# Performance work log

Measured on AMD Instinct MI355X. Metric: run time of the kernel, lower is better.

## Reference

```python
import jax, jax.numpy as jnp
import numpy as np

B, C, H, W = 8, 3840, 32, 32
C8 = C // 8


def setup_inputs() -> dict:
    key = jax.random.key(0)
    ks = jax.random.split(key, 4)
    x = jax.random.normal(ks[0], (B, C, H, W), dtype=jnp.float32)
    Wq = jax.random.normal(ks[1], (C8, C), dtype=jnp.float32) * 0.02
    Wk = jax.random.normal(ks[2], (C8, C), dtype=jnp.float32) * 0.02
    Wv = jax.random.normal(ks[3], (C, C), dtype=jnp.float32) * 0.02
    bq = jnp.zeros((C8,), jnp.float32)
    bk = jnp.zeros((C8,), jnp.float32)
    bv = jnp.zeros((C,), jnp.float32)
    gamma = jnp.zeros((1,), jnp.float32)
    return {"x": x, "Wq": Wq, "bq": bq, "Wk": Wk, "bk": bk,
            "Wv": Wv, "bv": bv, "gamma": gamma}


def reference(x, Wq, bq, Wk, bk, Wv, bv, gamma):
    b, c, h, w = x.shape
    n = h * w
    xf = x.reshape(b, c, n)  # flatten spatial: (B, C, N)
    # 1x1 convs == per-pixel channel matmuls
    q = jnp.einsum('oc,bcn->bon', Wq, xf) + bq[None, :, None]   # (B, C/8, N)
    k = jnp.einsum('oc,bcn->bon', Wk, xf) + bk[None, :, None]   # (B, C/8, N)
    v = jnp.einsum('oc,bcn->bon', Wv, xf) + bv[None, :, None]   # (B, C,  N)
    # energy[b,i,j] = q[b,:,i] . k[b,:,j]  (no scaling, as in source)
    energy = jnp.einsum('bci,bcj->bij', q, k)                    # (B, N, N)
    attn = jax.nn.softmax(energy, axis=-1)
    # out[b,c,i] = sum_j v[b,c,j] * attn[b,i,j]
    out = jnp.einsum('bcj,bij->bci', v, attn).reshape(b, c, h, w)
    return out * gamma + x
```

## Files before the change

kernel.cpp:

```cpp
#include <hip/hip_runtime.h>
#include <stdint.h>


typedef __attribute__((ext_vector_type(4))) float f32x4;
typedef __attribute__((ext_vector_type(8))) short bf16x8;
typedef __attribute__((ext_vector_type(4))) short s16x4;

namespace {
constexpr int kB = 8, kC = 3840, kC8 = 480, kN = 1024;
constexpr int kM  = 4800;
constexpr int kMp = 4864;
constexpr int kNT = kB * kN;
}

__device__ __forceinline__ short f2bf(float f) {
    union { float f; uint32_t u; } v; v.f = f;
    return (short)((v.u + 0x7FFFu + ((v.u >> 16) & 1u)) >> 16);
}

__device__ __forceinline__ void gl16(const void* g, void* l) {
    __builtin_amdgcn_global_load_lds(
        (const __attribute__((address_space(1))) void*)g,
        (__attribute__((address_space(3))) void*)(uint32_t)(uintptr_t)l,
        16, 0, 0);
}

#define DSR(d, a, o) asm volatile("ds_read_b128 %0, %1 offset:" o \
    : "=v"(d) : "v"(a) : "memory")

__global__ __launch_bounds__(256)
void convert_wc(const float* __restrict__ Wq, const float* __restrict__ Wk,
                const float* __restrict__ Wv, short* __restrict__ Wc)
{
    const size_t g  = (size_t)blockIdx.x * 256 + threadIdx.x;
    const size_t e0 = g * 8;
    const int r = (int)(e0 / kC);
    const int c = (int)(e0 % kC);
    const float* src = nullptr;
    if (r < kC8)          src = Wq + (size_t)r * kC + c;
    else if (r < 2 * kC8) src = Wk + (size_t)(r - kC8) * kC + c;
    else if (r < kM)      src = Wv + (size_t)(r - 2 * kC8) * kC + c;
    bf16x8 o;
    if (src) {
        float4 a = *(const float4*)src;
        float4 b = *(const float4*)(src + 4);
        o[0]=f2bf(a.x); o[1]=f2bf(a.y); o[2]=f2bf(a.z); o[3]=f2bf(a.w);
        o[4]=f2bf(b.x); o[5]=f2bf(b.y); o[6]=f2bf(b.z); o[7]=f2bf(b.w);
    } else {
        o = (bf16x8)0;
    }
    *(bf16x8*)(Wc + e0) = o;
}

__global__ __launch_bounds__(256)
void convert_bias(const float* __restrict__ bq, const float* __restrict__ bk,
                  const float* __restrict__ bv, float* __restrict__ biasC)
{
    const int r = blockIdx.x * 256 + threadIdx.x;
    if (r >= kMp) return;
    biasC[r] = r < kC8 ? bq[r] : r < 2*kC8 ? bk[r - kC8] : r < kM ? bv[r - 2*kC8] : 0.f;
}

__global__ __launch_bounds__(256)
void transpose_x(const float* __restrict__ x, short* __restrict__ xbT)
{
    __shared__ float t[32][33];
    const int tid = threadIdx.x;
    const int b = blockIdx.z, c0 = blockIdx.y * 32, n0 = blockIdx.x * 32;
    const int r = tid >> 3, q4 = (tid & 7) * 4;
    float4 v = *(const float4*)(x + ((size_t)b * kC + c0 + r) * kN + n0 + q4);
    t[r][q4] = v.x; t[r][q4+1] = v.y; t[r][q4+2] = v.z; t[r][q4+3] = v.w;
    __syncthreads();
    s16x4 o;
    o[0] = f2bf(t[q4+0][r]); o[1] = f2bf(t[q4+1][r]);
    o[2] = f2bf(t[q4+2][r]); o[3] = f2bf(t[q4+3][r]);
    *(s16x4*)(xbT + (size_t)(b * kN + n0 + r) * kC + c0 + q4) = o;
}

__global__ __launch_bounds__(256)
void transpose_qk(const short* __restrict__ qkv, short* __restrict__ qT,
                  short* __restrict__ kT)
{
    __shared__ short t[32][36];
    const int tid = threadIdx.x;
    const int o0 = blockIdx.y * 32, bn0 = blockIdx.x * 32;
    const int r = tid >> 3, q4 = (tid & 7) * 4;
    s16x4 v = *(const s16x4*)(qkv + (size_t)(o0 + r) * kNT + bn0 + q4);
    t[r][q4] = v[0]; t[r][q4+1] = v[1]; t[r][q4+2] = v[2]; t[r][q4+3] = v[3];
    __syncthreads();
    s16x4 o;
    o[0] = t[q4+0][r]; o[1] = t[q4+1][r]; o[2] = t[q4+2][r]; o[3] = t[q4+3][r];
    const int oc = o0 + q4;
    short* dst = (o0 < kC8) ? (qT + (size_t)(bn0 + r) * kC8 + oc)
                            : (kT + (size_t)(bn0 + r) * kC8 + (oc - kC8));
    *(s16x4*)dst = o;
}

__global__ __launch_bounds__(256) void gemm_bt_e(
    const short* __restrict__ Abase, int lda,
    const short* __restrict__ Bbase, int ldb,
    int ksteps, long zsa, long zsb, long zso,
    float* __restrict__ eout)
{
    __shared__ __align__(16) short ldsA[128 * 32];
    __shared__ __align__(16) short ldsB[128 * 32];

    const int tid  = threadIdx.x;
    const int lane = tid & 63;
    const int w    = tid >> 6;
    const int m0 = blockIdx.y * 128;
    const int n0 = blockIdx.x * 128;
    const int z  = blockIdx.z;

    const char* Ab = (const char*)(Abase + (size_t)z * zsa);
    const char* Bb = (const char*)(Bbase + (size_t)z * zsb);
    const size_t ldab = (size_t)lda * 2, ldbb = (size_t)ldb * 2;

    const int srow  = w * 16 + (lane >> 2);
    const int scolb = (lane & 3) * 16;
    char* lA = (char*)ldsA;
    char* lB = (char*)ldsB;

    f32x4 acc[4][4];
#pragma unroll
    for (int i = 0; i < 4; ++i)
#pragma unroll
        for (int j = 0; j < 4; ++j) acc[i][j] = (f32x4)0.f;

    const int wm = (w >> 1) * 64, wn = (w & 1) * 64;
    const int fr = lane & 15;
    const int kb = (lane >> 4) * 16;

    for (int s = 0; s < ksteps; ++s) {
        const int k0b = s * 64;
        if (s) __syncthreads();
        gl16(Ab + (size_t)(m0 + srow)      * ldab + k0b + scolb, lA + w * 1024);
        gl16(Ab + (size_t)(m0 + 64 + srow) * ldab + k0b + scolb, lA + 4096 + w * 1024);
        gl16(Bb + (size_t)(n0 + srow)      * ldbb + k0b + scolb, lB + w * 1024);
        gl16(Bb + (size_t)(n0 + 64 + srow) * ldbb + k0b + scolb, lB + 4096 + w * 1024);
        __syncthreads();

        bf16x8 af[4], bfv[4];
#pragma unroll
        for (int f = 0; f < 4; ++f) {
            af[f]  = *(const bf16x8*)(lA + (wm + f * 16 + fr) * 64 + kb);
            bfv[f] = *(const bf16x8*)(lB + (wn + f * 16 + fr) * 64 + kb);
        }
#pragma unroll
        for (int fm = 0; fm < 4; ++fm)
#pragma unroll
            for (int fn = 0; fn < 4; ++fn)
                acc[fm][fn] = __builtin_amdgcn_mfma_f32_16x16x32_bf16(
                    af[fm], bfv[fn], acc[fm][fn], 0, 0, 0);
    }

    const int rbase = (lane >> 4) * 4;
    float* eb = eout + (size_t)z * zso;
#pragma unroll
    for (int fm = 0; fm < 4; ++fm)
#pragma unroll
        for (int fn = 0; fn < 4; ++fn)
#pragma unroll
            for (int r = 0; r < 4; ++r)
                eb[(size_t)(m0 + wm + fm*16 + rbase + r) * kN + (n0 + wn + fn*16 + fr)]
                    = acc[fm][fn][r];
}

template<int MODE>
__global__ __launch_bounds__(512) void gemm256(
    const short* __restrict__ Abase, int lda,
    const short* __restrict__ Bbase, int ldb,
    int ksteps, int nxt, int nyt, long zsa, long zsb, long zso,
    short* __restrict__ qkv, const float* __restrict__ biasC,
    const float* __restrict__ x, const float* __restrict__ gamma,
    float* __restrict__ out)
{
    __shared__ __align__(16) char lds[131072];

    const int tid  = threadIdx.x;
    const int lane = tid & 63;
    const int w    = tid >> 6;

    const int nwg = (int)gridDim.x;
    const int id  = (int)blockIdx.x;
    const int q8 = nwg >> 3, r8g = nwg & 7;
    const int xcd = id & 7, pos = id >> 3;
    const int sw = (xcd < r8g ? xcd * (q8 + 1) : r8g * (q8 + 1) + (xcd - r8g) * q8) + pos;

    int m0, n0, bz;
    if (MODE == 0) {
        m0 = (sw / nyt) * 256;
        n0 = (sw % nyt) * 256;
        bz = 0;
    } else {
        bz = sw / (nxt * nyt);
        const int rem = sw % (nxt * nyt);
        n0 = (rem / nxt) * 256;
        m0 = (rem % nxt) * 256;
    }

    const char* Ab = (const char*)(Abase + (size_t)bz * zsa);
    const char* Bb = (const char*)(Bbase + (size_t)bz * zsb);
    const size_t ldab = (size_t)lda * 2, ldbb = (size_t)ldb * 2;

    const int r8  = tid >> 3;
    const int scb = ((tid & 7) * 16) ^ ((r8 & 7) << 4);

#define STAGE(S, SLOTBASE)                                                     \
    do {                                                                       \
        const size_t kb_ = (size_t)(S) * 128;                                  \
        _Pragma("unroll")                                                      \
        for (int i_ = 0; i_ < 4; ++i_)                                         \
            gl16(Ab + (size_t)(m0 + r8 + 64 * i_) * ldab + kb_ + scb,          \
                 (SLOTBASE) + i_ * 8192 + w * 1024);                           \
        _Pragma("unroll")                                                      \
        for (int i_ = 0; i_ < 4; ++i_)                                         \
            gl16(Bb + (size_t)(n0 + r8 + 64 * i_) * ldbb + kb_ + scb,          \
                 (SLOTBASE) + 32768 + i_ * 8192 + w * 1024);                   \
    } while (0)

    const uint32_t lbase = (uint32_t)(uintptr_t)&lds[0];
    const int wr = w >> 2, wc = w & 3;
    const int fr = lane & 15, kq = lane >> 4;
    const uint32_t xorv = (uint32_t)((fr & 7) << 4);
    const uint32_t aoff0 = (uint32_t)((wr*128 + fr) * 128) + (((uint32_t)(kq*16)) ^ xorv);
    const uint32_t aoff1 = (uint32_t)((wr*128 + fr) * 128) + (((uint32_t)(64 + kq*16)) ^ xorv);
    const uint32_t boff0 = 32768u + (uint32_t)((wc*64 + fr) * 128) + (((uint32_t)(kq*16)) ^ xorv);
    const uint32_t boff1 = 32768u + (uint32_t)((wc*64 + fr) * 128) + (((uint32_t)(64 + kq*16)) ^ xorv);

    f32x4 acc[8][4];
#pragma unroll
    for (int i = 0; i < 8; ++i)
#pragma unroll
        for (int j = 0; j < 4; ++j) acc[i][j] = (f32x4)0.f;

    STAGE(0, lds);
    STAGE(1, lds + 65536);

    const int ns = ksteps;
    for (int s = 0; s < ns; ++s) {
        const uint32_t cur = (uint32_t)(s & 1);
        if (s + 1 < ns) asm volatile("s_waitcnt vmcnt(8)" ::: "memory");
        else            asm volatile("s_waitcnt vmcnt(0)" ::: "memory");
        __builtin_amdgcn_sched_barrier(0);
        __builtin_amdgcn_s_barrier();
        __builtin_amdgcn_sched_barrier(0);

        const uint32_t sb = lbase + cur * 65536u;
        const uint32_t aa0 = sb + aoff0, aa1 = sb + aoff1;
        const uint32_t bb0 = sb + boff0, bb1 = sb + boff1;

        bf16x8 b0v[4], b1v[4], a0[8], a1[8];
        DSR(b0v[0], bb0, "0");    DSR(b0v[1], bb0, "2048");
        DSR(b0v[2], bb0, "4096"); DSR(b0v[3], bb0, "6144");
        DSR(b1v[0], bb1, "0");    DSR(b1v[1], bb1, "2048");
        DSR(b1v[2], bb1, "4096"); DSR(b1v[3], bb1, "6144");
        DSR(a0[0], aa0, "0");    DSR(a0[1], aa0, "2048");
        DSR(a1[0], aa1, "0");    DSR(a1[1], aa1, "2048");
        DSR(a0[2], aa0, "4096"); DSR(a0[3], aa0, "6144");
        DSR(a1[2], aa1, "4096"); DSR(a1[3], aa1, "6144");

        asm volatile("s_waitcnt lgkmcnt(4)" ::: "memory");
        __builtin_amdgcn_sched_barrier(0);
        __builtin_amdgcn_s_setprio(1);
#pragma unroll
        for (int fm = 0; fm < 2; ++fm)
#pragma unroll
            for (int fn = 0; fn < 4; ++fn) {
                acc[fm][fn] = __builtin_amdgcn_mfma_f32_16x16x32_bf16(a0[fm], b0v[fn], acc[fm][fn], 0, 0, 0);
                acc[fm][fn] = __builtin_amdgcn_mfma_f32_16x16x32_bf16(a1[fm], b1v[fn], acc[fm][fn], 0, 0, 0);
            }
        __builtin_amdgcn_s_setprio(0);

        DSR(a0[4], aa0, "8192"); DSR(a0[5], aa0, "10240");
        DSR(a1[4], aa1, "8192"); DSR(a1[5], aa1, "10240");
        asm volatile("s_waitcnt lgkmcnt(4)" ::: "memory");
        __builtin_amdgcn_sched_barrier(0);
        __builtin_amdgcn_s_setprio(1);
#pragma unroll
        for (int fm = 2; fm < 4; ++fm)
#pragma unroll
            for (int fn = 0; fn < 4; ++fn) {
                acc[fm][fn] = __builtin_amdgcn_mfma_f32_16x16x32_bf16(a0[fm], b0v[fn], acc[fm][fn], 0, 0, 0);
                acc[fm][fn] = __builtin_amdgcn_mfma_f32_16x16x32_bf16(a1[fm], b1v[fn], acc[fm][fn], 0, 0, 0);
            }
        __builtin_amdgcn_s_setprio(0);

        DSR(a0[6], aa0, "12288"); DSR(a0[7], aa0, "14336");
        DSR(a1[6], aa1, "12288"); DSR(a1[7], aa1, "14336");
        asm volatile("s_waitcnt lgkmcnt(4)" ::: "memory");
        __builtin_amdgcn_sched_barrier(0);
        __builtin_amdgcn_s_setprio(1);
#pragma unroll
        for (int fm = 4; fm < 6; ++fm)
#pragma unroll
            for (int fn = 0; fn < 4; ++fn) {
                acc[fm][fn] = __builtin_amdgcn_mfma_f32_16x16x32_bf16(a0[fm], b0v[fn], acc[fm][fn], 0, 0, 0);
                acc[fm][fn] = __builtin_amdgcn_mfma_f32_16x16x32_bf16(a1[fm], b1v[fn], acc[fm][fn], 0, 0, 0);
            }
        __builtin_amdgcn_s_setprio(0);

        asm volatile("s_waitcnt lgkmcnt(0)" ::: "memory");
        __builtin_amdgcn_sched_barrier(0);
        __builtin_amdgcn_s_barrier();
        __builtin_amdgcn_sched_barrier(0);

        if (s + 2 < ns)
            STAGE(s + 2, lds + cur * 65536);
        __builtin_amdgcn_sched_barrier(0);

        __builtin_amdgcn_s_setprio(1);
#pragma unroll
        for (int fm = 6; fm < 8; ++fm)
#pragma unroll
            for (int fn = 0; fn < 4; ++fn) {
                acc[fm][fn] = __builtin_amdgcn_mfma_f32_16x16x32_bf16(a0[fm], b0v[fn], acc[fm][fn], 0, 0, 0);
                acc[fm][fn] = __builtin_amdgcn_mfma_f32_16x16x32_bf16(a1[fm], b1v[fn], acc[fm][fn], 0, 0, 0);
            }
        __builtin_amdgcn_s_setprio(0);
    }
#undef STAGE

    const int rbase = kq * 4;
    if (MODE == 0) {
#pragma unroll
        for (int fm = 0; fm < 8; ++fm) {
#pragma unroll
            for (int rr = 0; rr < 4; ++rr) {
                const int gm = m0 + wr * 128 + fm * 16 + rbase + rr;
                if (gm < kM) {
                    const float bias = biasC[gm];
#pragma unroll
                    for (int fn = 0; fn < 4; ++fn) {
                        const int gn = n0 + wc * 64 + fn * 16 + fr;
                        qkv[(size_t)gm * kNT + gn] = f2bf(acc[fm][fn][rr] + bias);
                    }
                }
            }
        }
    } else {
        const float g = gamma[0];
        const float* xb = x + (size_t)bz * zso;
        float* ob = out + (size_t)bz * zso;
#pragma unroll
        for (int fm = 0; fm < 8; ++fm)
#pragma unroll
            for (int fn = 0; fn < 4; ++fn)
#pragma unroll
                for (int rr = 0; rr < 4; ++rr) {
                    const size_t idx = (size_t)(m0 + wr*128 + fm*16 + rbase + rr) * kN
                                     + (n0 + wc*64 + fn*16 + fr);
                    ob[idx] = g * acc[fm][fn][rr] + xb[idx];
                }
    }
}

__global__ __launch_bounds__(256)
void softmax_bf(const float* __restrict__ e, short* __restrict__ attnb)
{
    const int i = blockIdx.x, b = blockIdx.y, tid = threadIdx.x;
    const float* row = e + ((size_t)b * kN + i) * kN;

    float4 vv = *(const float4*)(row + tid * 4);
    float m = fmaxf(fmaxf(vv.x, vv.y), fmaxf(vv.z, vv.w));

    __shared__ float red[8];
#pragma unroll
    for (int off = 32; off > 0; off >>= 1)
        m = fmaxf(m, __shfl_down(m, off));
    if ((tid & 63) == 0) red[tid >> 6] = m;
    __syncthreads();
    m = fmaxf(fmaxf(red[0], red[1]), fmaxf(red[2], red[3]));

    float e0 = expf(vv.x - m), e1 = expf(vv.y - m);
    float e2 = expf(vv.z - m), e3 = expf(vv.w - m);
    float s = e0 + e1 + e2 + e3;
#pragma unroll
    for (int off = 32; off > 0; off >>= 1)
        s += __shfl_down(s, off);
    if ((tid & 63) == 0) red[4 + (tid >> 6)] = s;
    __syncthreads();
    s = red[4] + red[5] + red[6] + red[7];

    const float inv = 1.0f / s;
    s16x4 o;
    o[0] = f2bf(e0 * inv); o[1] = f2bf(e1 * inv);
    o[2] = f2bf(e2 * inv); o[3] = f2bf(e3 * inv);
    *(s16x4*)(attnb + ((size_t)b * kN + i) * kN + tid * 4) = o;
}

extern "C" void kernel_launch(void* const* d_in, const int* in_sizes, int n_in,
                              void* d_out, int out_size, void* d_ws, size_t ws_size,
                              hipStream_t stream) {
    const float* x     = (const float*)d_in[0];
    const float* Wq    = (const float*)d_in[1];
    const float* bq    = (const float*)d_in[2];
    const float* Wk    = (const float*)d_in[3];
    const float* bk    = (const float*)d_in[4];
    const float* Wv    = (const float*)d_in[5];
    const float* bv    = (const float*)d_in[6];
    const float* gamma = (const float*)d_in[7];
    float* out = (float*)d_out;

    char* base = (char*)d_ws;
    short* xbT   = (short*)(base);
    short* attnb = (short*)(base);
    short* qT    = (short*)(base + 16777216);
    short* kT    = (short*)(base + 24641536);
    short* Wc    = (short*)(base + 62914560);
    float* attnf = (float*)(base + 62914560);
    float* biasC = (float*)(base + 100270080);
    short* qkv   = (short*)(base + 100289536);

    convert_wc  <<<9120, 256, 0, stream>>>(Wq, Wk, Wv, Wc);
    convert_bias<<<19, 256, 0, stream>>>(bq, bk, bv, biasC);
    transpose_x <<<dim3(32, 120, 8), 256, 0, stream>>>(x, xbT);

    gemm256<0><<<608, 512, 0, stream>>>(
        Wc, kC, xbT, kC, kC / 64, 19, 32, 0, 0, 0,
        qkv, biasC, nullptr, nullptr, nullptr);

    transpose_qk<<<dim3(256, 30, 1), 256, 0, stream>>>(qkv, qT, kT);

    gemm_bt_e<<<dim3(8, 8, 8), 256, 0, stream>>>(
        qT, kC8, kT, kC8, kC8 / 32,
        (long)kN * kC8, (long)kN * kC8, (long)kN * kN, attnf);

    softmax_bf<<<dim3(kN, kB), 256, 0, stream>>>(attnf, attnb);

    gemm256<2><<<480, 512, 0, stream>>>(
        qkv + (size_t)960 * kNT, kNT, attnb, kN, kN / 64, 15, 4,
        (long)kN, (long)kN * kN, (long)kC * kN,
        nullptr, nullptr, x, gamma, out);
}
```

Before: 536.3 us.

## Restructure GEMM main loop into four-phase ping-pong schedule with split A/B staging

```diff
diff --git a/kernel.cpp b/kernel.cpp
--- a/kernel.cpp
+++ b/kernel.cpp
@@ -206,13 +206,17 @@
     const int r8  = tid >> 3;
     const int scb = ((tid & 7) * 16) ^ ((r8 & 7) << 4);
 
-#define STAGE(S, SLOTBASE)                                                     \
+#define STAGE_A(S, SLOTBASE)                                                   \
     do {                                                                       \
         const size_t kb_ = (size_t)(S) * 128;                                  \
         _Pragma("unroll")                                                      \
         for (int i_ = 0; i_ < 4; ++i_)                                         \
             gl16(Ab + (size_t)(m0 + r8 + 64 * i_) * ldab + kb_ + scb,          \
                  (SLOTBASE) + i_ * 8192 + w * 1024);                           \
+    } while (0)
+#define STAGE_B(S, SLOTBASE)                                                   \
+    do {                                                                       \
+        const size_t kb_ = (size_t)(S) * 128;                                  \
         _Pragma("unroll")                                                      \
         for (int i_ = 0; i_ < 4; ++i_)                                         \
             gl16(Bb + (size_t)(n0 + r8 + 64 * i_) * ldbb + kb_ + scb,          \
@@ -234,92 +238,95 @@
 #pragma unroll
         for (int j = 0; j < 4; ++j) acc[i][j] = (f32x4)0.f;
 
-    STAGE(0, lds);
-    STAGE(1, lds + 65536);
+    STAGE_A(0, lds);           STAGE_B(0, lds);
+    STAGE_A(1, lds + 65536);   STAGE_B(1, lds + 65536);
+    asm volatile("s_waitcnt vmcnt(8)" ::: "memory");
+    __builtin_amdgcn_s_barrier();
 
     const int ns = ksteps;
     for (int s = 0; s < ns; ++s) {
-        const uint32_t cur = (uint32_t)(s & 1);
-        if (s + 1 < ns) asm volatile("s_waitcnt vmcnt(8)" ::: "memory");
-        else            asm volatile("s_waitcnt vmcnt(0)" ::: "memory");
-        __builtin_amdgcn_sched_barrier(0);
-        __builtin_amdgcn_s_barrier();
-        __builtin_amdgcn_sched_barrier(0);
-
-        const uint32_t sb = lbase + cur * 65536u;
+        const uint32_t sb = lbase + (uint32_t)(s & 1) * 65536u;
         const uint32_t aa0 = sb + aoff0, aa1 = sb + aoff1;
         const uint32_t bb0 = sb + boff0, bb1 = sb + boff1;
-
-        bf16x8 b0v[4], b1v[4], a0[8], a1[8];
-        DSR(b0v[0], bb0, "0");    DSR(b0v[1], bb0, "2048");
-        DSR(b0v[2], bb0, "4096"); DSR(b0v[3], bb0, "6144");
-        DSR(b1v[0], bb1, "0");    DSR(b1v[1], bb1, "2048");
-        DSR(b1v[2], bb1, "4096"); DSR(b1v[3], bb1, "6144");
+        char* const slotb = lds + (s & 1) * 65536;
+
+        bf16x8 a0[8], a1[8], b0v[4], b1v[4];
+
         DSR(a0[0], aa0, "0");    DSR(a0[1], aa0, "2048");
+        DSR(a0[2], aa0, "4096"); DSR(a0[3], aa0, "6144");
         DSR(a1[0], aa1, "0");    DSR(a1[1], aa1, "2048");
-        DSR(a0[2], aa0, "4096"); DSR(a0[3], aa0, "6144");
         DSR(a1[2], aa1, "4096"); DSR(a1[3], aa1, "6144");
-
-        asm volatile("s_waitcnt lgkmcnt(4)" ::: "memory");
+        DSR(b0v[0], bb0, "0");   DSR(b0v[1], bb0, "2048");
+        DSR(b1v[0], bb1, "0");   DSR(b1v[1], bb1, "2048");
+        __builtin_amdgcn_s_barrier();
+        asm volatile("s_waitcnt lgkmcnt(0)" ::: "memory");
         __builtin_amdgcn_sched_barrier(0);
         __builtin_amdgcn_s_setprio(1);
 #pragma unroll
-        for (int fm = 0; fm < 2; ++fm)
-#pragma unroll
-            for (int fn = 0; fn < 4; ++fn) {
+        for (int fm = 0; fm < 4; ++fm)
+#pragma unroll
+            for (int fn = 0; fn < 2; ++fn) {
                 acc[fm][fn] = __builtin_amdgcn_mfma_f32_16x16x32_bf16(a0[fm], b0v[fn], acc[fm][fn], 0, 0, 0);
                 acc[fm][fn] = __builtin_amdgcn_mfma_f32_16x16x32_bf16(a1[fm], b1v[fn], acc[fm][fn], 0, 0, 0);
             }
         __builtin_amdgcn_s_setprio(0);
-
-        DSR(a0[4], aa0, "8192"); DSR(a0[5], aa0, "10240");
-        DSR(a1[4], aa1, "8192"); DSR(a1[5], aa1, "10240");
-        asm volatile("s_waitcnt lgkmcnt(4)" ::: "memory");
+        __builtin_amdgcn_s_barrier();
+
+        DSR(b0v[2], bb0, "4096"); DSR(b0v[3], bb0, "6144");
+        DSR(b1v[2], bb1, "4096"); DSR(b1v[3], bb1, "6144");
+        __builtin_amdgcn_s_barrier();
+        asm volatile("s_waitcnt lgkmcnt(0)" ::: "memory");
         __builtin_amdgcn_sched_barrier(0);
         __builtin_amdgcn_s_setprio(1);
 #pragma unroll
-        for (int fm = 2; fm < 4; ++fm)
-#pragma unroll
-            for (int fn = 0; fn < 4; ++fn) {
+        for (int fm = 0; fm < 4; ++fm)
+#pragma unroll
+            for (int fn = 2; fn < 4; ++fn) {
                 acc[fm][fn] = __builtin_amdgcn_mfma_f32_16x16x32_bf16(a0[fm], b0v[fn], acc[fm][fn], 0, 0, 0);
                 acc[fm][fn] = __builtin_amdgcn_mfma_f32_16x16x32_bf16(a1[fm], b1v[fn], acc[fm][fn], 0, 0, 0);
             }
         __builtin_amdgcn_s_setprio(0);
-
+        __builtin_amdgcn_s_barrier();
+
+        DSR(a0[4], aa0, "8192");  DSR(a0[5], aa0, "10240");
         DSR(a0[6], aa0, "12288"); DSR(a0[7], aa0, "14336");
+        DSR(a1[4], aa1, "8192");  DSR(a1[5], aa1, "10240");
         DSR(a1[6], aa1, "12288"); DSR(a1[7], aa1, "14336");
-        asm volatile("s_waitcnt lgkmcnt(4)" ::: "memory");
+        if (s + 2 < ns) STAGE_B(s + 2, slotb);
+        __builtin_amdgcn_s_barrier();
+        asm volatile("s_waitcnt lgkmcnt(0)" ::: "memory");
         __builtin_amdgcn_sched_barrier(0);
         __builtin_amdgcn_s_setprio(1);
 #pragma unroll
-        for (int fm = 4; fm < 6; ++fm)
-#pragma unroll
-            for (int fn = 0; fn < 4; ++fn) {
+        for (int fm = 4; fm < 8; ++fm)
+#pragma unroll
+            for (int fn = 2; fn < 4; ++fn) {
                 acc[fm][fn] = __builtin_amdgcn_mfma_f32_16x16x32_bf16(a0[fm], b0v[fn], acc[fm][fn], 0, 0, 0);
                 acc[fm][fn] = __builtin_amdgcn_mfma_f32_16x16x32_bf16(a1[fm], b1v[fn], acc[fm][fn], 0, 0, 0);
             }
         __builtin_amdgcn_s_setprio(0);
-
-        asm volatile("s_waitcnt lgkmcnt(0)" ::: "memory");
+        __builtin_amdgcn_s_barrier();
+
+        if (s + 2 < ns) STAGE_A(s + 2, slotb);
+        if (s + 1 < ns) {
+            if (s + 2 < ns) asm volatile("s_waitcnt vmcnt(8)" ::: "memory");
+            else            asm volatile("s_waitcnt vmcnt(0)" ::: "memory");
+        }
         __builtin_amdgcn_sched_barrier(0);
         __builtin_amdgcn_s_barrier();
-        __builtin_amdgcn_sched_barrier(0);
-
-        if (s + 2 < ns)
-            STAGE(s + 2, lds + cur * 65536);
-        __builtin_amdgcn_sched_barrier(0);
-
         __builtin_amdgcn_s_setprio(1);
 #pragma unroll
-        for (int fm = 6; fm < 8; ++fm)
-#pragma unroll
-            for (int fn = 0; fn < 4; ++fn) {
+        for (int fm = 4; fm < 8; ++fm)
+#pragma unroll
+            for (int fn = 0; fn < 2; ++fn) {
                 acc[fm][fn] = __builtin_amdgcn_mfma_f32_16x16x32_bf16(a0[fm], b0v[fn], acc[fm][fn], 0, 0, 0);
                 acc[fm][fn] = __builtin_amdgcn_mfma_f32_16x16x32_bf16(a1[fm], b1v[fn], acc[fm][fn], 0, 0, 0);
             }
         __builtin_amdgcn_s_setprio(0);
+        __builtin_amdgcn_s_barrier();
     }
-#undef STAGE
+#undef STAGE_A
+#undef STAGE_B
 
     const int rbase = kq * 4;
     if (MODE == 0) {
```

Result: no change. 530.8 us (-1.0%).

## Replace hand-scheduled LDS reads with plain loads in GEMM main loop

Applied to the files above, without the earlier changes.

```diff
diff --git a/kernel.cpp b/kernel.cpp
--- a/kernel.cpp
+++ b/kernel.cpp
@@ -24,9 +24,6 @@
         (__attribute__((address_space(3))) void*)(uint32_t)(uintptr_t)l,
         16, 0, 0);
 }
-
-#define DSR(d, a, o) asm volatile("ds_read_b128 %0, %1 offset:" o \
-    : "=v"(d) : "v"(a) : "memory")
 
 __global__ __launch_bounds__(256)
 void convert_wc(const float* __restrict__ Wq, const float* __restrict__ Wk,
@@ -219,7 +216,6 @@
                  (SLOTBASE) + 32768 + i_ * 8192 + w * 1024);                   \
     } while (0)
 
-    const uint32_t lbase = (uint32_t)(uintptr_t)&lds[0];
     const int wr = w >> 2, wc = w & 3;
     const int fr = lane & 15, kq = lane >> 4;
     const uint32_t xorv = (uint32_t)((fr & 7) << 4);
@@ -239,85 +235,39 @@
 
     const int ns = ksteps;
     for (int s = 0; s < ns; ++s) {
-        const uint32_t cur = (uint32_t)(s & 1);
         if (s + 1 < ns) asm volatile("s_waitcnt vmcnt(8)" ::: "memory");
         else            asm volatile("s_waitcnt vmcnt(0)" ::: "memory");
+        __builtin_amdgcn_s_barrier();
+
+        const char* sb = lds + (size_t)(s & 1) * 65536;
+        __builtin_amdgcn_s_setprio(1);
+
+        bf16x8 a0[8], a1[8], b0v[4], b1v[4];
+#pragma unroll
+        for (int f = 0; f < 4; ++f) {
+            b0v[f] = *(const bf16x8*)(sb + boff0 + f * 2048);
+            b1v[f] = *(const bf16x8*)(sb + boff1 + f * 2048);
+        }
+#pragma unroll
+        for (int f = 0; f < 8; ++f) {
+            a0[f] = *(const bf16x8*)(sb + aoff0 + f * 2048);
+            a1[f] = *(const bf16x8*)(sb + aoff1 + f * 2048);
+        }
+#pragma unroll
+        for (int fm = 0; fm < 8; ++fm)
+#pragma unroll
+            for (int fn = 0; fn < 4; ++fn) {
+                acc[fm][fn] = __builtin_amdgcn_mfma_f32_16x16x32_bf16(
+                    a0[fm], b0v[fn], acc[fm][fn], 0, 0, 0);
+                acc[fm][fn] = __builtin_amdgcn_mfma_f32_16x16x32_bf16(
+                    a1[fm], b1v[fn], acc[fm][fn], 0, 0, 0);
+            }
+        __builtin_amdgcn_s_setprio(0);
+
         __builtin_amdgcn_sched_barrier(0);
         __builtin_amdgcn_s_barrier();
-        __builtin_amdgcn_sched_barrier(0);
-
-        const uint32_t sb = lbase + cur * 65536u;
-        const uint32_t aa0 = sb + aoff0, aa1 = sb + aoff1;
-        const uint32_t bb0 = sb + boff0, bb1 = sb + boff1;
-
-        bf16x8 b0v[4], b1v[4], a0[8], a1[8];
-        DSR(b0v[0], bb0, "0");    DSR(b0v[1], bb0, "2048");
-        DSR(b0v[2], bb0, "4096"); DSR(b0v[3], bb0, "6144");
-        DSR(b1v[0], bb1, "0");    DSR(b1v[1], bb1, "2048");
-        DSR(b1v[2], bb1, "4096"); DSR(b1v[3], bb1, "6144");
-        DSR(a0[0], aa0, "0");    DSR(a0[1], aa0, "2048");
-        DSR(a1[0], aa1, "0");    DSR(a1[1], aa1, "2048");
-        DSR(a0[2], aa0, "4096"); DSR(a0[3], aa0, "6144");
-        DSR(a1[2], aa1, "4096"); DSR(a1[3], aa1, "6144");
-
-        asm volatile("s_waitcnt lgkmcnt(4)" ::: "memory");
-        __builtin_amdgcn_sched_barrier(0);
-        __builtin_amdgcn_s_setprio(1);
-#pragma unroll
-        for (int fm = 0; fm < 2; ++fm)
-#pragma unroll
-            for (int fn = 0; fn < 4; ++fn) {
-                acc[fm][fn] = __builtin_amdgcn_mfma_f32_16x16x32_bf16(a0[fm], b0v[fn], acc[fm][fn], 0, 0, 0);
-                acc[fm][fn] = __builtin_amdgcn_mfma_f32_16x16x32_bf16(a1[fm], b1v[fn], acc[fm][fn], 0, 0, 0);
-            }
-        __builtin_amdgcn_s_setprio(0);
-
-        DSR(a0[4], aa0, "8192"); DSR(a0[5], aa0, "10240");
-        DSR(a1[4], aa1, "8192"); DSR(a1[5], aa1, "10240");
-        asm volatile("s_waitcnt lgkmcnt(4)" ::: "memory");
-        __builtin_amdgcn_sched_barrier(0);
-        __builtin_amdgcn_s_setprio(1);
-#pragma unroll
-        for (int fm = 2; fm < 4; ++fm)
-#pragma unroll
-            for (int fn = 0; fn < 4; ++fn) {
-                acc[fm][fn] = __builtin_amdgcn_mfma_f32_16x16x32_bf16(a0[fm], b0v[fn], acc[fm][fn], 0, 0, 0);
-                acc[fm][fn] = __builtin_amdgcn_mfma_f32_16x16x32_bf16(a1[fm], b1v[fn], acc[fm][fn], 0, 0, 0);
-            }
-        __builtin_amdgcn_s_setprio(0);
-
-        DSR(a0[6], aa0, "12288"); DSR(a0[7], aa0, "14336");
-        DSR(a1[6], aa1, "12288"); DSR(a1[7], aa1, "14336");
-        asm volatile("s_waitcnt lgkmcnt(4)" ::: "memory");
-        __builtin_amdgcn_sched_barrier(0);
-        __builtin_amdgcn_s_setprio(1);
-#pragma unroll
-        for (int fm = 4; fm < 6; ++fm)
-#pragma unroll
-            for (int fn = 0; fn < 4; ++fn) {
-                acc[fm][fn] = __builtin_amdgcn_mfma_f32_16x16x32_bf16(a0[fm], b0v[fn], acc[fm][fn], 0, 0, 0);
-                acc[fm][fn] = __builtin_amdgcn_mfma_f32_16x16x32_bf16(a1[fm], b1v[fn], acc[fm][fn], 0, 0, 0);
-            }
-        __builtin_amdgcn_s_setprio(0);
-
-        asm volatile("s_waitcnt lgkmcnt(0)" ::: "memory");
-        __builtin_amdgcn_sched_barrier(0);
-        __builtin_amdgcn_s_barrier();
-        __builtin_amdgcn_sched_barrier(0);
-
         if (s + 2 < ns)
-            STAGE(s + 2, lds + cur * 65536);
-        __builtin_amdgcn_sched_barrier(0);
-
-        __builtin_amdgcn_s_setprio(1);
-#pragma unroll
-        for (int fm = 6; fm < 8; ++fm)
-#pragma unroll
-            for (int fn = 0; fn < 4; ++fn) {
-                acc[fm][fn] = __builtin_amdgcn_mfma_f32_16x16x32_bf16(a0[fm], b0v[fn], acc[fm][fn], 0, 0, 0);
-                acc[fm][fn] = __builtin_amdgcn_mfma_f32_16x16x32_bf16(a1[fm], b1v[fn], acc[fm][fn], 0, 0, 0);
-            }
-        __builtin_amdgcn_s_setprio(0);
+            STAGE(s + 2, lds + (size_t)(s & 1) * 65536);
     }
 #undef STAGE
 
```

New measurement: 571.8 us. 1.07x slower.
